# Optimization experiments

Hardware: AMD Instinct MI355X
Metric: run time of the kernel (lower is better)

The kernel has to match this reference:

```python
import jax, jax.numpy as jnp
import numpy as np

# Dims: B=4096 batch, E=8 experts, D=1024 in, H=4096 hidden, O=1024 out.
# Faithful to MoE.forward in training mode: every expert runs on every sample,
# then outputs are combined weighted by softmax gating probabilities.

def setup_inputs() -> dict:
    key = jax.random.key(0)
    ks = jax.random.split(key, 5)
    B, E, D, H, O = 4096, 8, 1024, 4096, 1024
    x = jax.random.normal(ks[0], (B, D), dtype=jnp.float32)
    W1 = jax.random.normal(ks[1], (E, D, H), dtype=jnp.float32) * (1.0 / np.sqrt(D))
    b1 = jnp.zeros((E, H), dtype=jnp.float32)
    W2 = jax.random.normal(ks[2], (E, H, O), dtype=jnp.float32) * (1.0 / np.sqrt(H))
    b2 = jnp.zeros((E, O), dtype=jnp.float32)
    Wg = jax.random.normal(ks[3], (D, E), dtype=jnp.float32) * (1.0 / np.sqrt(D))
    bg = jnp.zeros((E,), dtype=jnp.float32)
    return {"x": x, "W1": W1, "b1": b1, "W2": W2, "b2": b2, "Wg": Wg, "bg": bg}


def reference(x, W1, b1, W2, b2, Wg, bg):
    # gating_net(x.view(B, -1)) -> softmax probabilities [B, E]
    gating_probs = jax.nn.softmax(x @ Wg + bg, axis=-1)
    # expert_outputs = stack([student(x) for student in students], dim=1) -> [B, E, O]
    h = jax.nn.relu(jnp.einsum('bd,edh->beh', x, W1) + b1)  # [B, E, H]
    expert_outputs = jnp.einsum('beh,eho->beo', h, W2) + b2  # [B, E, O]
    # weighted combine: (expert_outputs * probs[..., None]).sum(dim=1)
    outputs = jnp.einsum('beo,be->bo', expert_outputs, gating_probs)  # [B, O]
    return outputs
```

## Files before the change

### kernel.cpp

```cpp
#include <hip/hip_runtime.h>
#include <hip/hip_bf16.h>


#define B_DIM 4096
#define E_DIM 8
#define D_DIM 1024
#define H_DIM 4096
#define O_DIM 1024
#define KTOT  (E_DIM * H_DIM)
#define KSPLIT 4

typedef __attribute__((ext_vector_type(8))) short bf16x8;
typedef __attribute__((ext_vector_type(4))) float f32x4;

__device__ __forceinline__ unsigned short f2bf(float f) {
  union { float f; unsigned u; } c; c.f = f;
  unsigned r = c.u + 0x7fffu + ((c.u >> 16) & 1u);
  return (unsigned short)(r >> 16);
}

__device__ __forceinline__ void gload_lds16(const void* g, void* l) {
  __builtin_amdgcn_global_load_lds(
      (const __attribute__((address_space(1))) void*)g,
      (__attribute__((address_space(3))) void*)l, 16, 0, 0);
}

__device__ __forceinline__ void barfence() {
  asm volatile("" ::: "memory");
  __builtin_amdgcn_s_barrier();
  asm volatile("" ::: "memory");
}

__device__ __forceinline__ unsigned swzA(unsigned o) {
  return o ^ (((o >> 7) & 7u) << 4);
}

__device__ __forceinline__ void stageHalf(const char* gbase, size_t rowBytes, int kByte,
                                          char* seg, int tid) {
  #pragma unroll
  for (int r = 0; r < 2; ++r) {
    unsigned o = (unsigned)((r * 512 + tid) * 16);
    unsigned q = swzA(o);
    gload_lds16(gbase + (size_t)(q >> 7) * rowBytes + kByte + (q & 127), seg + o);
  }
}

template<bool STAGE, int VMN>
__device__ __forceinline__ void tile4(
    char* smem, int bufOff,
    const char* AbC, const char* BbC, size_t rbA, size_t rbB, int kStage,
    int wm, int wn, int lane, int tid, f32x4 (&acc)[8][4])
{
  bf16x8 aF[4][2], bLo[2][2], bHi[2][2];
  const char* aSeg = smem + bufOff + wm * 16384;
  const char* bSeg = smem + bufOff + (2 + (wn >> 1)) * 16384;

  #pragma unroll
  for (int m = 0; m < 4; ++m)
    #pragma unroll
    for (int kk = 0; kk < 2; ++kk) {
      unsigned o = (unsigned)((m * 16 + (lane & 15)) * 128 + kk * 64 + ((lane >> 4) * 16));
      aF[m][kk] = *(const bf16x8*)(aSeg + swzA(o));
    }
  #pragma unroll
  for (int n = 0; n < 2; ++n)
    #pragma unroll
    for (int kk = 0; kk < 2; ++kk) {
      unsigned o = (unsigned)(((wn & 1) * 64 + n * 16 + (lane & 15)) * 128 + kk * 64 + ((lane >> 4) * 16));
      bLo[n][kk] = *(const bf16x8*)(bSeg + swzA(o));
    }
  asm volatile("s_waitcnt lgkmcnt(8)" ::: "memory");
  barfence();
  asm volatile("s_waitcnt lgkmcnt(0)" ::: "memory");
  __builtin_amdgcn_s_setprio(1);
  #pragma unroll
  for (int m = 0; m < 4; ++m)
    #pragma unroll
    for (int n = 0; n < 2; ++n)
      #pragma unroll
      for (int kk = 0; kk < 2; ++kk)
        acc[m][n] = __builtin_amdgcn_mfma_f32_16x16x32_bf16(aF[m][kk], bLo[n][kk], acc[m][n], 0, 0, 0);
  __builtin_amdgcn_s_setprio(0);
  barfence();

  #pragma unroll
  for (int n = 0; n < 2; ++n)
    #pragma unroll
    for (int kk = 0; kk < 2; ++kk) {
      unsigned o = (unsigned)(((wn & 1) * 64 + (2 + n) * 16 + (lane & 15)) * 128 + kk * 64 + ((lane >> 4) * 16));
      bHi[n][kk] = *(const bf16x8*)(bSeg + swzA(o));
    }
  barfence();
  asm volatile("s_waitcnt lgkmcnt(0)" ::: "memory");
  __builtin_amdgcn_s_setprio(1);
  #pragma unroll
  for (int m = 0; m < 4; ++m)
    #pragma unroll
    for (int n = 0; n < 2; ++n)
      #pragma unroll
      for (int kk = 0; kk < 2; ++kk)
        acc[m][2 + n] = __builtin_amdgcn_mfma_f32_16x16x32_bf16(aF[m][kk], bHi[n][kk], acc[m][2 + n], 0, 0, 0);
  __builtin_amdgcn_s_setprio(0);
  barfence();

  #pragma unroll
  for (int m = 0; m < 4; ++m)
    #pragma unroll
    for (int kk = 0; kk < 2; ++kk) {
      unsigned o = (unsigned)(((4 + m) * 16 + (lane & 15)) * 128 + kk * 64 + ((lane >> 4) * 16));
      aF[m][kk] = *(const bf16x8*)(aSeg + swzA(o));
    }
  if (STAGE) {
    stageHalf(BbC,                    rbB, kStage, smem + bufOff + 2 * 16384, tid);
    stageHalf(BbC + (size_t)128 * rbB, rbB, kStage, smem + bufOff + 3 * 16384, tid);
  }
  barfence();
  asm volatile("s_waitcnt lgkmcnt(0)" ::: "memory");
  __builtin_amdgcn_s_setprio(1);
  #pragma unroll
  for (int m = 0; m < 4; ++m)
    #pragma unroll
    for (int n = 0; n < 2; ++n)
      #pragma unroll
      for (int kk = 0; kk < 2; ++kk)
        acc[4 + m][2 + n] = __builtin_amdgcn_mfma_f32_16x16x32_bf16(aF[m][kk], bHi[n][kk], acc[4 + m][2 + n], 0, 0, 0);
  __builtin_amdgcn_s_setprio(0);
  barfence();

  if (STAGE) {
    stageHalf(AbC,                    rbA, kStage, smem + bufOff + 0,     tid);
    stageHalf(AbC + (size_t)128 * rbA, rbA, kStage, smem + bufOff + 16384, tid);
  }
  if (VMN == 8)      asm volatile("s_waitcnt vmcnt(8)" ::: "memory");
  else if (VMN == 0) asm volatile("s_waitcnt vmcnt(0)" ::: "memory");
  barfence();
  __builtin_amdgcn_s_setprio(1);
  #pragma unroll
  for (int m = 0; m < 4; ++m)
    #pragma unroll
    for (int n = 0; n < 2; ++n)
      #pragma unroll
      for (int kk = 0; kk < 2; ++kk)
        acc[4 + m][n] = __builtin_amdgcn_mfma_f32_16x16x32_bf16(aF[m][kk], bLo[n][kk], acc[4 + m][n], 0, 0, 0);
  __builtin_amdgcn_s_setprio(0);
  barfence();
}

template<int MODE>
__global__ __launch_bounds__(512, 2)
void gemm8p(const unsigned short* __restrict__ A,
            const unsigned short* __restrict__ Bt,
            void* __restrict__ Cout,
            const float* __restrict__ probs,
            const float* __restrict__ bias,
            int M, int N, int K, int kChunk)
{
  __shared__ __align__(16) char smem[131072];

  const int tid = threadIdx.x;
  const int wave = tid >> 6, lane = tid & 63;
  const int wm = wave >> 2, wn = wave & 3;

  int mt, nt, kBeg;
  if (MODE == 1) {
    int bid = blockIdx.x;
    int xcd = bid & 7, seq = bid >> 3;
    int grp = seq >> 4, g = seq & 15;
    mt = (grp & 3) * 4 + (g & 3);
    nt = xcd * 16 + (grp >> 2) * 4 + (g >> 2);
    kBeg = 0;
  } else {
    int x = blockIdx.x;
    mt = (x & 7) * 2 + ((x >> 3) & 1);
    nt = x >> 4;
    kBeg = blockIdx.y * kChunk;
  }

  const char* AbC = (const char*)(A + (size_t)mt * 256 * K);
  const char* BbC = (const char*)(Bt + (size_t)nt * 256 * K);
  const size_t rbA = (size_t)K * 2, rbB = (size_t)K * 2;

  f32x4 acc[8][4] = {};

  const int NT = kChunk / 64;
  const int NI = NT / 2;

  {
    int k0 = kBeg * 2, k1 = (kBeg + 64) * 2;
    stageHalf(BbC,                    rbB, k0, smem + 2 * 16384, tid);
    stageHalf(BbC + (size_t)128 * rbB, rbB, k0, smem + 3 * 16384, tid);
    stageHalf(AbC,                    rbA, k0, smem + 0,         tid);
    stageHalf(AbC + (size_t)128 * rbA, rbA, k0, smem + 16384,    tid);
    stageHalf(BbC,                    rbB, k1, smem + 65536 + 2 * 16384, tid);
    stageHalf(BbC + (size_t)128 * rbB, rbB, k1, smem + 65536 + 3 * 16384, tid);
    stageHalf(AbC,                    rbA, k1, smem + 65536 + 0,         tid);
    stageHalf(AbC + (size_t)128 * rbA, rbA, k1, smem + 65536 + 16384,    tid);
  }
  asm volatile("s_waitcnt vmcnt(8)" ::: "memory");
  barfence();

  for (int i = 0; i < NI - 1; ++i) {
    int ks0 = (kBeg + (2 * i + 2) * 64) * 2;
    int ks1 = (kBeg + (2 * i + 3) * 64) * 2;
    tile4<true, 8>(smem, 0,     AbC, BbC, rbA, rbB, ks0, wm, wn, lane, tid, acc);
    tile4<true, 8>(smem, 65536, AbC, BbC, rbA, rbB, ks1, wm, wn, lane, tid, acc);
  }
  tile4<false, 0>(smem, 0,     AbC, BbC, rbA, rbB, 0, wm, wn, lane, tid, acc);
  tile4<false, -1>(smem, 65536, AbC, BbC, rbA, rbB, 0, wm, wn, lane, tid, acc);

  const int colBase = nt * 256 + wn * 64;
  const int rowBase = mt * 256 + wm * 128;
  #pragma unroll
  for (int m = 0; m < 8; ++m) {
    #pragma unroll
    for (int n = 0; n < 4; ++n) {
      const int col = colBase + n * 16 + (lane & 15);
      #pragma unroll
      for (int j = 0; j < 4; ++j) {
        const int row = rowBase + m * 16 + ((lane >> 4) * 4) + j;
        float v = acc[m][n][j];
        if (MODE == 1) {
          v += bias[col];
          v = fmaxf(v, 0.0f) * probs[row * E_DIM + (col >> 12)];
          ((unsigned short*)Cout)[(size_t)row * N + col] = f2bf(v);
        } else {
          float* dst = (float*)Cout + (size_t)blockIdx.y * M * N;
          dst[(size_t)row * N + col] = v;
        }
      }
    }
  }
}

__global__ __launch_bounds__(256) void gating_kernel(
    const float* __restrict__ x, const float* __restrict__ Wg,
    const float* __restrict__ bg, float* __restrict__ probs)
{
  __shared__ float sWg[D_DIM * E_DIM];
  for (int i = threadIdx.x; i < D_DIM * E_DIM; i += 256) sWg[i] = Wg[i];
  __syncthreads();

  const int wave = threadIdx.x >> 6, lane = threadIdx.x & 63;
  const int b = blockIdx.x * 4 + wave;

  float acc[E_DIM] = {};
  const float* xr = x + (size_t)b * D_DIM;
  #pragma unroll
  for (int i = 0; i < D_DIM / 64; ++i) {
    int d = i * 64 + lane;
    float xv = xr[d];
    #pragma unroll
    for (int e = 0; e < E_DIM; ++e) acc[e] += xv * sWg[d * E_DIM + e];
  }
  #pragma unroll
  for (int e = 0; e < E_DIM; ++e) {
    #pragma unroll
    for (int off = 32; off > 0; off >>= 1) acc[e] += __shfl_down(acc[e], off);
  }
  if (lane == 0) {
    float m = -1e30f;
    #pragma unroll
    for (int e = 0; e < E_DIM; ++e) { acc[e] += bg[e]; m = fmaxf(m, acc[e]); }
    float p[E_DIM]; float s = 0.f;
    #pragma unroll
    for (int e = 0; e < E_DIM; ++e) { p[e] = expf(acc[e] - m); s += p[e]; }
    float inv = 1.0f / s;
    #pragma unroll
    for (int e = 0; e < E_DIM; ++e) probs[(size_t)b * E_DIM + e] = p[e] * inv;
  }
}

__global__ __launch_bounds__(256) void convert_x_kernel(
    const float* __restrict__ x, unsigned short* __restrict__ xb)
{
  int i = blockIdx.x * 256 + threadIdx.x;
  const float4* src = (const float4*)x;
  float4 v = src[i];
  union { unsigned short u[4]; unsigned long long q; } o;
  o.u[0] = f2bf(v.x); o.u[1] = f2bf(v.y); o.u[2] = f2bf(v.z); o.u[3] = f2bf(v.w);
  *(unsigned long long*)(xb + (size_t)i * 4) = o.q;
}

__global__ __launch_bounds__(256) void transpose_w1(
    const float* __restrict__ W1, unsigned short* __restrict__ W1t)
{
  __shared__ float t[32][33];
  const int e = blockIdx.z;
  const int d0 = blockIdx.y * 32;
  const int h0 = blockIdx.x * 32;
  const int tx = threadIdx.x & 31, ty = threadIdx.x >> 5;
  const float* src = W1 + (size_t)e * D_DIM * H_DIM;
  #pragma unroll
  for (int i = 0; i < 4; ++i)
    t[ty + 8 * i][tx] = src[(size_t)(d0 + ty + 8 * i) * H_DIM + h0 + tx];
  __syncthreads();
  #pragma unroll
  for (int i = 0; i < 4; ++i)
    W1t[((size_t)e * H_DIM + h0 + ty + 8 * i) * D_DIM + d0 + tx] =
        f2bf(t[tx][ty + 8 * i]);
}

__global__ __launch_bounds__(256) void transpose_w2(
    const float* __restrict__ W2, unsigned short* __restrict__ W2t)
{
  __shared__ float t[32][33];
  const int e = blockIdx.z;
  const int h0 = blockIdx.y * 32;
  const int o0 = blockIdx.x * 32;
  const int tx = threadIdx.x & 31, ty = threadIdx.x >> 5;
  const float* src = W2 + (size_t)e * H_DIM * O_DIM;
  #pragma unroll
  for (int i = 0; i < 4; ++i)
    t[ty + 8 * i][tx] = src[(size_t)(h0 + ty + 8 * i) * O_DIM + o0 + tx];
  __syncthreads();
  #pragma unroll
  for (int i = 0; i < 4; ++i)
    W2t[(size_t)(o0 + ty + 8 * i) * KTOT + (size_t)e * H_DIM + h0 + tx] =
        f2bf(t[tx][ty + 8 * i]);
}

__global__ __launch_bounds__(256) void reduce_out(
    const float* __restrict__ partial, const float* __restrict__ probs,
    const float* __restrict__ b2, float* __restrict__ out)
{
  const int i = blockIdx.x * 256 + threadIdx.x;
  const int row = i >> 8;
  const int colv = i & 255;
  const size_t plane = (size_t)B_DIM * O_DIM / 4;

  float4 v = make_float4(0.f, 0.f, 0.f, 0.f);
  #pragma unroll
  for (int ks = 0; ks < KSPLIT; ++ks) {
    float4 p = ((const float4*)partial)[ks * plane + i];
    v.x += p.x; v.y += p.y; v.z += p.z; v.w += p.w;
  }
  #pragma unroll
  for (int e = 0; e < E_DIM; ++e) {
    float pe = probs[row * E_DIM + e];
    float4 b = ((const float4*)b2)[e * (O_DIM / 4) + colv];
    v.x += pe * b.x; v.y += pe * b.y; v.z += pe * b.z; v.w += pe * b.w;
  }
  ((float4*)out)[i] = v;
}

extern "C" void kernel_launch(void* const* d_in, const int* in_sizes, int n_in,
                              void* d_out, int out_size, void* d_ws, size_t ws_size,
                              hipStream_t stream)
{
  const float* x  = (const float*)d_in[0];
  const float* W1 = (const float*)d_in[1];
  const float* b1 = (const float*)d_in[2];
  const float* W2 = (const float*)d_in[3];
  const float* b2 = (const float*)d_in[4];
  const float* Wg = (const float*)d_in[5];
  const float* bg = (const float*)d_in[6];
  float* out = (float*)d_out;

  char* ws = (char*)d_ws;
  float*          probs = (float*)ws;
  unsigned short* xb    = (unsigned short*)(ws + (1u << 17));
  unsigned short* W1t   = (unsigned short*)(ws + (1u << 17) + (8u << 20));
  unsigned short* W2t   = (unsigned short*)(ws + (1u << 17) + (8u << 20) + (64u << 20));
  unsigned short* hp    = (unsigned short*)(ws + (1u << 17) + (8u << 20) + (128u << 20));
  float* partial = (float*)W1t;

  gating_kernel<<<B_DIM / 4, 256, 0, stream>>>(x, Wg, bg, probs);
  convert_x_kernel<<<(B_DIM * D_DIM / 4) / 256, 256, 0, stream>>>(x, xb);
  transpose_w1<<<dim3(H_DIM / 32, D_DIM / 32, E_DIM), 256, 0, stream>>>(W1, W1t);
  transpose_w2<<<dim3(O_DIM / 32, H_DIM / 32, E_DIM), 256, 0, stream>>>(W2, W2t);

  gemm8p<1><<<dim3((B_DIM / 256) * (KTOT / 256), 1), 512, 0, stream>>>(
      xb, W1t, hp, probs, b1, B_DIM, KTOT, D_DIM, D_DIM);

  gemm8p<2><<<dim3((B_DIM / 256) * (O_DIM / 256), KSPLIT), 512, 0, stream>>>(
      hp, W2t, partial, probs, nullptr, B_DIM, O_DIM, KTOT, KTOT / KSPLIT);

  reduce_out<<<(B_DIM * O_DIM / 4) / 256, 256, 0, stream>>>(partial, probs, b2, out);
}
```

Measured before the change: 980.4 us.

## Software-pipeline LDS fragment loads across k-tiles and widen weight transpose tiles

Restructures the GEMM inner loop so the A/B register fragments for the next k-tile are loaded from LDS during the current tile's MFMAs. Barriers are reduced and sched_barrier pins the instruction order. The goal is to hide LDS read latency behind matrix math. The two weight transpose kernels are merged into one generic kernel with 64x64 tiles and packed 8-byte bf16 stores, which should cut memory transactions in preprocessing. The deeper pipeline holds more live fragment registers and leans on subtler barrier and waitcnt ordering, so it risks a race or register spills.

New measurement: 1.398 ms. +42.6%, slower.

```diff
diff --git a/kernel.cpp b/kernel.cpp
--- a/kernel.cpp
+++ b/kernel.cpp
@@ -13,6 +13,8 @@
 typedef __attribute__((ext_vector_type(8))) short bf16x8;
 typedef __attribute__((ext_vector_type(4))) float f32x4;
 
+#define SCHED0 __builtin_amdgcn_sched_barrier(0)
+
 __device__ __forceinline__ unsigned short f2bf(float f) {
   union { float f; unsigned u; } c; c.f = f;
   unsigned r = c.u + 0x7fffu + ((c.u >> 16) & 1u);
@@ -45,105 +47,120 @@
   }
 }
 
-template<bool STAGE, int VMN>
-__device__ __forceinline__ void tile4(
-    char* smem, int bufOff,
-    const char* AbC, const char* BbC, size_t rbA, size_t rbB, int kStage,
-    int wm, int wn, int lane, int tid, f32x4 (&acc)[8][4])
-{
-  bf16x8 aF[4][2], bLo[2][2], bHi[2][2];
-  const char* aSeg = smem + bufOff + wm * 16384;
-  const char* bSeg = smem + bufOff + (2 + (wn >> 1)) * 16384;
+__device__ __forceinline__ bf16x8 ldsA(const char* aSeg, int m, int kk, int lane) {
+  unsigned o = (unsigned)((m * 16 + (lane & 15)) * 128 + kk * 64 + ((lane >> 4) * 16));
+  return *(const bf16x8*)(aSeg + swzA(o));
+}
+__device__ __forceinline__ bf16x8 ldsB(const char* bSeg, int wn, int n, int kk, int lane) {
+  unsigned o = (unsigned)(((wn & 1) * 64 + n * 16 + (lane & 15)) * 128 + kk * 64 + ((lane >> 4) * 16));
+  return *(const bf16x8*)(bSeg + swzA(o));
+}
+
+template<bool STAGE, bool PIPE, int VMN>
+__device__ __forceinline__ void tileK(
+    char* smem, int cur,
+    const char* AbC, const char* BbC, size_t rb, int kStage,
+    int wm, int wn, int lane, int tid,
+    bf16x8 (&aLo)[4][2], bf16x8 (&aHi)[4][2],
+    bf16x8 (&bLo)[2][2], bf16x8 (&bHi)[2][2],
+    f32x4 (&acc)[8][4])
+{
+  char* bufC = smem + cur * 65536;
+  char* bufN = smem + (cur ^ 1) * 65536;
+  const char* aSegC = bufC + wm * 16384;
+  const char* bSegC = bufC + (2 + (wn >> 1)) * 16384;
+  const char* aSegN = bufN + wm * 16384;
+  const char* bSegN = bufN + (2 + (wn >> 1)) * 16384;
+
+  #pragma unroll
+  for (int n = 0; n < 2; ++n)
+    #pragma unroll
+    for (int kk = 0; kk < 2; ++kk)
+      bHi[n][kk] = ldsB(bSegC, wn, 2 + n, kk, lane);
+  SCHED0;
+  __builtin_amdgcn_s_setprio(1);
+  #pragma unroll
+  for (int kk = 0; kk < 2; ++kk)
+    #pragma unroll
+    for (int m = 0; m < 4; ++m)
+      #pragma unroll
+      for (int n = 0; n < 2; ++n)
+        acc[m][n] = __builtin_amdgcn_mfma_f32_16x16x32_bf16(aLo[m][kk], bLo[n][kk], acc[m][n], 0, 0, 0);
+  __builtin_amdgcn_s_setprio(0);
+  SCHED0;
 
   #pragma unroll
   for (int m = 0; m < 4; ++m)
     #pragma unroll
-    for (int kk = 0; kk < 2; ++kk) {
-      unsigned o = (unsigned)((m * 16 + (lane & 15)) * 128 + kk * 64 + ((lane >> 4) * 16));
-      aF[m][kk] = *(const bf16x8*)(aSeg + swzA(o));
-    }
-  #pragma unroll
-  for (int n = 0; n < 2; ++n)
-    #pragma unroll
-    for (int kk = 0; kk < 2; ++kk) {
-      unsigned o = (unsigned)(((wn & 1) * 64 + n * 16 + (lane & 15)) * 128 + kk * 64 + ((lane >> 4) * 16));
-      bLo[n][kk] = *(const bf16x8*)(bSeg + swzA(o));
-    }
-  asm volatile("s_waitcnt lgkmcnt(8)" ::: "memory");
+    for (int kk = 0; kk < 2; ++kk)
+      aHi[m][kk] = ldsA(aSegC, 4 + m, kk, lane);
+  SCHED0;
+  __builtin_amdgcn_s_setprio(1);
+  #pragma unroll
+  for (int kk = 0; kk < 2; ++kk)
+    #pragma unroll
+    for (int m = 0; m < 4; ++m)
+      #pragma unroll
+      for (int n = 0; n < 2; ++n)
+        acc[m][2 + n] = __builtin_amdgcn_mfma_f32_16x16x32_bf16(aLo[m][kk], bHi[n][kk], acc[m][2 + n], 0, 0, 0);
+  __builtin_amdgcn_s_setprio(0);
+  SCHED0;
   barfence();
-  asm volatile("s_waitcnt lgkmcnt(0)" ::: "memory");
+
+  if (STAGE) {
+    stageHalf(BbC,                     rb, kStage, bufC + 2 * 16384, tid);
+    stageHalf(BbC + (size_t)128 * rb,  rb, kStage, bufC + 3 * 16384, tid);
+  }
+  SCHED0;
+  if (VMN >= 0) {
+    if (VMN == 4) asm volatile("s_waitcnt vmcnt(4)" ::: "memory");
+    else          asm volatile("s_waitcnt vmcnt(0)" ::: "memory");
+    barfence();
+  }
+  SCHED0;
+  if (PIPE) {
+    #pragma unroll
+    for (int m = 0; m < 4; ++m)
+      #pragma unroll
+      for (int kk = 0; kk < 2; ++kk)
+        aLo[m][kk] = ldsA(aSegN, m, kk, lane);
+  }
+  SCHED0;
   __builtin_amdgcn_s_setprio(1);
   #pragma unroll
-  for (int m = 0; m < 4; ++m)
+  for (int kk = 0; kk < 2; ++kk)
+    #pragma unroll
+    for (int m = 0; m < 4; ++m)
+      #pragma unroll
+      for (int n = 0; n < 2; ++n)
+        acc[4 + m][n] = __builtin_amdgcn_mfma_f32_16x16x32_bf16(aHi[m][kk], bLo[n][kk], acc[4 + m][n], 0, 0, 0);
+  __builtin_amdgcn_s_setprio(0);
+  SCHED0;
+  barfence();
+
+  SCHED0;
+  if (PIPE) {
     #pragma unroll
     for (int n = 0; n < 2; ++n)
       #pragma unroll
       for (int kk = 0; kk < 2; ++kk)
-        acc[m][n] = __builtin_amdgcn_mfma_f32_16x16x32_bf16(aF[m][kk], bLo[n][kk], acc[m][n], 0, 0, 0);
+        bLo[n][kk] = ldsB(bSegN, wn, n, kk, lane);
+  }
+  if (STAGE) {
+    stageHalf(AbC,                     rb, kStage, bufC + 0,     tid);
+    stageHalf(AbC + (size_t)128 * rb,  rb, kStage, bufC + 16384, tid);
+  }
+  SCHED0;
+  __builtin_amdgcn_s_setprio(1);
+  #pragma unroll
+  for (int kk = 0; kk < 2; ++kk)
+    #pragma unroll
+    for (int m = 0; m < 4; ++m)
+      #pragma unroll
+      for (int n = 0; n < 2; ++n)
+        acc[4 + m][2 + n] = __builtin_amdgcn_mfma_f32_16x16x32_bf16(aHi[m][kk], bHi[n][kk], acc[4 + m][2 + n], 0, 0, 0);
   __builtin_amdgcn_s_setprio(0);
-  barfence();
-
-  #pragma unroll
-  for (int n = 0; n < 2; ++n)
-    #pragma unroll
-    for (int kk = 0; kk < 2; ++kk) {
-      unsigned o = (unsigned)(((wn & 1) * 64 + (2 + n) * 16 + (lane & 15)) * 128 + kk * 64 + ((lane >> 4) * 16));
-      bHi[n][kk] = *(const bf16x8*)(bSeg + swzA(o));
-    }
-  barfence();
-  asm volatile("s_waitcnt lgkmcnt(0)" ::: "memory");
-  __builtin_amdgcn_s_setprio(1);
-  #pragma unroll
-  for (int m = 0; m < 4; ++m)
-    #pragma unroll
-    for (int n = 0; n < 2; ++n)
-      #pragma unroll
-      for (int kk = 0; kk < 2; ++kk)
-        acc[m][2 + n] = __builtin_amdgcn_mfma_f32_16x16x32_bf16(aF[m][kk], bHi[n][kk], acc[m][2 + n], 0, 0, 0);
-  __builtin_amdgcn_s_setprio(0);
-  barfence();
-
-  #pragma unroll
-  for (int m = 0; m < 4; ++m)
-    #pragma unroll
-    for (int kk = 0; kk < 2; ++kk) {
-      unsigned o = (unsigned)(((4 + m) * 16 + (lane & 15)) * 128 + kk * 64 + ((lane >> 4) * 16));
-      aF[m][kk] = *(const bf16x8*)(aSeg + swzA(o));
-    }
-  if (STAGE) {
-    stageHalf(BbC,                    rbB, kStage, smem + bufOff + 2 * 16384, tid);
-    stageHalf(BbC + (size_t)128 * rbB, rbB, kStage, smem + bufOff + 3 * 16384, tid);
-  }
-  barfence();
-  asm volatile("s_waitcnt lgkmcnt(0)" ::: "memory");
-  __builtin_amdgcn_s_setprio(1);
-  #pragma unroll
-  for (int m = 0; m < 4; ++m)
-    #pragma unroll
-    for (int n = 0; n < 2; ++n)
-      #pragma unroll
-      for (int kk = 0; kk < 2; ++kk)
-        acc[4 + m][2 + n] = __builtin_amdgcn_mfma_f32_16x16x32_bf16(aF[m][kk], bHi[n][kk], acc[4 + m][2 + n], 0, 0, 0);
-  __builtin_amdgcn_s_setprio(0);
-  barfence();
-
-  if (STAGE) {
-    stageHalf(AbC,                    rbA, kStage, smem + bufOff + 0,     tid);
-    stageHalf(AbC + (size_t)128 * rbA, rbA, kStage, smem + bufOff + 16384, tid);
-  }
-  if (VMN == 8)      asm volatile("s_waitcnt vmcnt(8)" ::: "memory");
-  else if (VMN == 0) asm volatile("s_waitcnt vmcnt(0)" ::: "memory");
-  barfence();
-  __builtin_amdgcn_s_setprio(1);
-  #pragma unroll
-  for (int m = 0; m < 4; ++m)
-    #pragma unroll
-    for (int n = 0; n < 2; ++n)
-      #pragma unroll
-      for (int kk = 0; kk < 2; ++kk)
-        acc[4 + m][n] = __builtin_amdgcn_mfma_f32_16x16x32_bf16(aF[m][kk], bLo[n][kk], acc[4 + m][n], 0, 0, 0);
-  __builtin_amdgcn_s_setprio(0);
-  barfence();
+  SCHED0;
 }
 
 template<int MODE>
@@ -178,35 +195,46 @@
 
   const char* AbC = (const char*)(A + (size_t)mt * 256 * K);
   const char* BbC = (const char*)(Bt + (size_t)nt * 256 * K);
-  const size_t rbA = (size_t)K * 2, rbB = (size_t)K * 2;
+  const size_t rb = (size_t)K * 2;
 
   f32x4 acc[8][4] = {};
+  bf16x8 aLo[4][2], aHi[4][2], bLo[2][2], bHi[2][2];
 
   const int NT = kChunk / 64;
-  const int NI = NT / 2;
 
   {
     int k0 = kBeg * 2, k1 = (kBeg + 64) * 2;
-    stageHalf(BbC,                    rbB, k0, smem + 2 * 16384, tid);
-    stageHalf(BbC + (size_t)128 * rbB, rbB, k0, smem + 3 * 16384, tid);
-    stageHalf(AbC,                    rbA, k0, smem + 0,         tid);
-    stageHalf(AbC + (size_t)128 * rbA, rbA, k0, smem + 16384,    tid);
-    stageHalf(BbC,                    rbB, k1, smem + 65536 + 2 * 16384, tid);
-    stageHalf(BbC + (size_t)128 * rbB, rbB, k1, smem + 65536 + 3 * 16384, tid);
-    stageHalf(AbC,                    rbA, k1, smem + 65536 + 0,         tid);
-    stageHalf(AbC + (size_t)128 * rbA, rbA, k1, smem + 65536 + 16384,    tid);
+    stageHalf(BbC,                    rb, k0, smem + 2 * 16384, tid);
+    stageHalf(BbC + (size_t)128 * rb, rb, k0, smem + 3 * 16384, tid);
+    stageHalf(AbC,                    rb, k0, smem + 0,         tid);
+    stageHalf(AbC + (size_t)128 * rb, rb, k0, smem + 16384,     tid);
+    stageHalf(BbC,                    rb, k1, smem + 65536 + 2 * 16384, tid);
+    stageHalf(BbC + (size_t)128 * rb, rb, k1, smem + 65536 + 3 * 16384, tid);
+    stageHalf(AbC,                    rb, k1, smem + 65536 + 0,         tid);
+    stageHalf(AbC + (size_t)128 * rb, rb, k1, smem + 65536 + 16384,     tid);
   }
   asm volatile("s_waitcnt vmcnt(8)" ::: "memory");
   barfence();
-
-  for (int i = 0; i < NI - 1; ++i) {
-    int ks0 = (kBeg + (2 * i + 2) * 64) * 2;
-    int ks1 = (kBeg + (2 * i + 3) * 64) * 2;
-    tile4<true, 8>(smem, 0,     AbC, BbC, rbA, rbB, ks0, wm, wn, lane, tid, acc);
-    tile4<true, 8>(smem, 65536, AbC, BbC, rbA, rbB, ks1, wm, wn, lane, tid, acc);
-  }
-  tile4<false, 0>(smem, 0,     AbC, BbC, rbA, rbB, 0, wm, wn, lane, tid, acc);
-  tile4<false, -1>(smem, 65536, AbC, BbC, rbA, rbB, 0, wm, wn, lane, tid, acc);
+  SCHED0;
+  #pragma unroll
+  for (int m = 0; m < 4; ++m)
+    #pragma unroll
+    for (int kk = 0; kk < 2; ++kk)
+      aLo[m][kk] = ldsA(smem + wm * 16384, m, kk, lane);
+  #pragma unroll
+  for (int n = 0; n < 2; ++n)
+    #pragma unroll
+    for (int kk = 0; kk < 2; ++kk)
+      bLo[n][kk] = ldsB(smem + (2 + (wn >> 1)) * 16384, wn, n, kk, lane);
+  SCHED0;
+
+  for (int t = 0; t < NT - 2; ++t)
+    tileK<true, true, 4>(smem, t & 1, AbC, BbC, rb, (kBeg + (t + 2) * 64) * 2,
+                         wm, wn, lane, tid, aLo, aHi, bLo, bHi, acc);
+  tileK<false, true, 0>(smem, (NT - 2) & 1, AbC, BbC, rb, 0,
+                        wm, wn, lane, tid, aLo, aHi, bLo, bHi, acc);
+  tileK<false, false, -1>(smem, (NT - 1) & 1, AbC, BbC, rb, 0,
+                          wm, wn, lane, tid, aLo, aHi, bLo, bHi, acc);
 
   const int colBase = nt * 256 + wn * 64;
   const int rowBase = mt * 256 + wm * 128;
@@ -281,42 +309,36 @@
   *(unsigned long long*)(xb + (size_t)i * 4) = o.q;
 }
 
-__global__ __launch_bounds__(256) void transpose_w1(
-    const float* __restrict__ W1, unsigned short* __restrict__ W1t)
-{
-  __shared__ float t[32][33];
+__global__ __launch_bounds__(256) void transpose_cvt(
+    const float* __restrict__ src, unsigned short* __restrict__ dst,
+    int ldSrc, int ldDst, size_t srcPlane, size_t dstPlane)
+{
+  __shared__ float t[64][65];
   const int e = blockIdx.z;
-  const int d0 = blockIdx.y * 32;
-  const int h0 = blockIdx.x * 32;
-  const int tx = threadIdx.x & 31, ty = threadIdx.x >> 5;
-  const float* src = W1 + (size_t)e * D_DIM * H_DIM;
-  #pragma unroll
-  for (int i = 0; i < 4; ++i)
-    t[ty + 8 * i][tx] = src[(size_t)(d0 + ty + 8 * i) * H_DIM + h0 + tx];
+  const int x0 = blockIdx.x * 64;
+  const int y0 = blockIdx.y * 64;
+  const float* s = src + (size_t)e * srcPlane;
+  unsigned short* d = dst + (size_t)e * dstPlane;
+
+  const int c = threadIdx.x & 63;
+  const int r4 = threadIdx.x >> 6;
+  #pragma unroll
+  for (int i = 0; i < 16; ++i) {
+    int r = r4 + 4 * i;
+    t[r][c] = s[(size_t)(x0 + r) * ldSrc + y0 + c];
+  }
   __syncthreads();
-  #pragma unroll
-  for (int i = 0; i < 4; ++i)
-    W1t[((size_t)e * H_DIM + h0 + ty + 8 * i) * D_DIM + d0 + tx] =
-        f2bf(t[tx][ty + 8 * i]);
-}
-
-__global__ __launch_bounds__(256) void transpose_w2(
-    const float* __restrict__ W2, unsigned short* __restrict__ W2t)
-{
-  __shared__ float t[32][33];
-  const int e = blockIdx.z;
-  const int h0 = blockIdx.y * 32;
-  const int o0 = blockIdx.x * 32;
-  const int tx = threadIdx.x & 31, ty = threadIdx.x >> 5;
-  const float* src = W2 + (size_t)e * H_DIM * O_DIM;
-  #pragma unroll
-  for (int i = 0; i < 4; ++i)
-    t[ty + 8 * i][tx] = src[(size_t)(h0 + ty + 8 * i) * O_DIM + o0 + tx];
-  __syncthreads();
-  #pragma unroll
-  for (int i = 0; i < 4; ++i)
-    W2t[(size_t)(o0 + ty + 8 * i) * KTOT + (size_t)e * H_DIM + h0 + tx] =
-        f2bf(t[tx][ty + 8 * i]);
+
+  const int x4 = (threadIdx.x & 15) * 4;
+  const int yb = threadIdx.x >> 4;
+  #pragma unroll
+  for (int j = 0; j < 4; ++j) {
+    int y = yb + 16 * j;
+    union { unsigned short u[4]; unsigned long long q; } o;
+    #pragma unroll
+    for (int q = 0; q < 4; ++q) o.u[q] = f2bf(t[x4 + q][y]);
+    *(unsigned long long*)(d + (size_t)(y0 + y) * ldDst + x0 + x4) = o.q;
+  }
 }
 
 __global__ __launch_bounds__(256) void reduce_out(
@@ -366,8 +388,10 @@
 
   gating_kernel<<<B_DIM / 4, 256, 0, stream>>>(x, Wg, bg, probs);
   convert_x_kernel<<<(B_DIM * D_DIM / 4) / 256, 256, 0, stream>>>(x, xb);
-  transpose_w1<<<dim3(H_DIM / 32, D_DIM / 32, E_DIM), 256, 0, stream>>>(W1, W1t);
-  transpose_w2<<<dim3(O_DIM / 32, H_DIM / 32, E_DIM), 256, 0, stream>>>(W2, W2t);
+  transpose_cvt<<<dim3(D_DIM / 64, H_DIM / 64, E_DIM), 256, 0, stream>>>(
+      W1, W1t, H_DIM, D_DIM, (size_t)D_DIM * H_DIM, (size_t)H_DIM * D_DIM);
+  transpose_cvt<<<dim3(H_DIM / 64, O_DIM / 64, E_DIM), 256, 0, stream>>>(
+      W2, W2t, O_DIM, KTOT, (size_t)H_DIM * O_DIM, (size_t)H_DIM);
 
   gemm8p<1><<<dim3((B_DIM / 256) * (KTOT / 256), 1), 512, 0, stream>>>(
       xb, W1t, hp, probs, b1, B_DIM, KTOT, D_DIM, D_DIM);
```
